# Kernel tuning notes

Measured on AMD Instinct MI355X. Metric: run time of the kernel, lower is better.

Reference implementation:

```python
import jax, jax.numpy as jnp
import numpy as np

B, T, HID = 2, 1024, 2048
H, DK, DV = 16, 128, 128
KC = 4          # short-conv kernel size
CHUNK = 64
EPS = 1e-5


def _dwconv_silu(x, w):
    # causal depthwise conv1d + SiLU: x [B,T,C], w [C,K]
    K = w.shape[1]
    xp = jnp.pad(x, ((0, 0), (K - 1, 0), (0, 0)))
    y = sum(xp[:, i:i + x.shape[1], :] * w[:, i] for i in range(K))
    return jax.nn.silu(y)


def _l2norm(x):
    return x * jax.lax.rsqrt(jnp.sum(x * x, -1, keepdims=True) + 1e-6)


def setup_inputs() -> dict:
    key = jax.random.key(0)
    ks = jax.random.split(key, 22)
    std = 0.02
    w = lambda k, s: jax.random.normal(k, s, jnp.float32) * std
    return dict(
        hidden_states=jax.random.normal(ks[0], (B, T, HID), jnp.float32),
        Wq=w(ks[1], (HID, H * DK)),
        Wk=w(ks[2], (HID, H * DK)),
        Wv=w(ks[3], (HID, H * DV)),
        conv_wq=w(ks[4], (H * DK, KC)),
        conv_wk=w(ks[5], (H * DK, KC)),
        conv_wv=w(ks[6], (H * DV, KC)),
        Wgb1=w(ks[7], (HID, DV)), Wgb2=w(ks[8], (DV, H * DK)),
        Wgd1=w(ks[9], (HID, DV)), Wgd2=w(ks[10], (DV, H * DK)),
        Wbb=w(ks[11], (HID, H)), Wbd=w(ks[12], (HID, H)),
        Wlam=w(ks[13], (HID, H)),
        A_log=jnp.log(jax.random.uniform(ks[14], (H,), jnp.float32, 1.0, 16.0)),
        dt_bias=jnp.zeros((H * DK,), jnp.float32),
        Wg1=w(ks[15], (HID, DV)), Wg2=w(ks[16], (DV, H * DV)),
        bg2=jnp.zeros((H * DV,), jnp.float32),
        onorm_w=jnp.ones((DV,), jnp.float32),
        Wo=w(ks[17], (H * DV, HID)),
    )


def _fkda_core(q, k, v, gf, gs, bf, bs):
    # dual-state (fast/slow) gated delta rule.
    # q,k: [B,T,H,DK]; v: [B,T,H,DV]; gf/gs: log-decay [B,T,H,DK]; bf/bs: [B,T,H]
    scale = DK ** -0.5
    tm = lambda x: jnp.moveaxis(x, 1, 0)                 # time-major
    qT, kT, vT = tm(q) * scale, tm(k), tm(v)
    g2 = jnp.stack([tm(gf), tm(gs)], 1)                  # [T,2,B,H,DK]
    b2 = jnp.stack([tm(bf), tm(bs)], 1)                  # [T,2,B,H]
    NC = T // CHUNK
    chunkify = lambda x: x.reshape((NC, CHUNK) + x.shape[1:])
    inputs = tuple(map(chunkify, (qT, kT, vT, g2, b2)))

    def step(S, inp):
        qt, kt, vt, gt, bt = inp                         # S: [2,B,H,DK,DV]
        S = S * jnp.exp(gt)[..., None]                   # per-channel decay on key dim
        mem = jnp.einsum('bhk,sbhkv->sbhv', kt, S)       # current memory readout
        u = bt[..., None] * (vt[None] - mem)             # delta-rule residual write
        S = S + jnp.einsum('bhk,sbhv->sbhkv', kt, u)
        o = jnp.einsum('bhk,sbhkv->sbhv', qt, S)
        return S, o

    @jax.checkpoint
    def chunk_step(S, inp):
        return jax.lax.scan(step, S, inp)

    S0 = jnp.zeros((2, q.shape[0], H, DK, DV), q.dtype)
    _, o = jax.lax.scan(chunk_step, S0, inputs)          # [NC,CHUNK,2,B,H,DV]
    o = o.reshape((T,) + o.shape[2:])
    return jnp.moveaxis(o[:, 0], 0, 1), jnp.moveaxis(o[:, 1], 0, 1)


def reference(hidden_states, Wq, Wk, Wv, conv_wq, conv_wk, conv_wv,
              Wgb1, Wgb2, Wgd1, Wgd2, Wbb, Wbd, Wlam, A_log, dt_bias,
              Wg1, Wg2, bg2, onorm_w, Wo):
    x = hidden_states
    b, t, _ = x.shape
    q = _dwconv_silu(x @ Wq, conv_wq).reshape(b, t, H, DK)
    k = _dwconv_silu(x @ Wk, conv_wk).reshape(b, t, H, DK)
    v = _dwconv_silu(x @ Wv, conv_wv).reshape(b, t, H, DV)
    g_base = ((x @ Wgb1) @ Wgb2).reshape(b, t, H, DK)    # low-rank decay gates
    g_delta = ((x @ Wgd1) @ Wgd2).reshape(b, t, H, DK)
    bb, bd = x @ Wbb, x @ Wbd
    lam = jax.nn.sigmoid(x @ Wlam)                       # [b,t,H] fast/slow mix
    beta_fast = jax.nn.sigmoid(bb + bd)
    beta_slow = jax.nn.sigmoid(bb - bd)
    dtb = dt_bias.reshape(H, DK)
    gate_of = lambda g: -jnp.exp(A_log)[None, None, :, None] * jax.nn.softplus(g + dtb)
    gf = gate_of(g_base + g_delta)                       # fused_kda_gate, fast
    gs = gate_of(g_base - g_delta)                       # slow (share_decay_gate=False)
    q, k = _l2norm(q), _l2norm(k)                        # use_qk_l2norm_in_kernel
    o_f, o_s = _fkda_core(q, k, v, gf, gs, beta_fast, beta_slow)
    o = lam[..., None] * o_f + (1.0 - lam[..., None]) * o_s
    gate = ((x @ Wg1) @ Wg2 + bg2).reshape(b, t, H, DV)
    o = o * jax.lax.rsqrt(jnp.mean(o * o, -1, keepdims=True) + EPS) * onorm_w
    o = o * jax.nn.sigmoid(gate)                         # FusedRMSNormGated(sigmoid)
    return o.reshape(b, t, H * DV) @ Wo
```

## Files before the change

kernel.cpp:

```cpp
#include <hip/hip_runtime.h>
#include <hip/hip_bf16.h>
#include <math.h>
#include <stdint.h>

#define B_   2
#define T_   1024
#define HID_ 2048
#define H_   16
#define DK_  128
#define DV_  128
#define TS_  16

typedef __bf16 bf16;
typedef __attribute__((ext_vector_type(8))) __bf16 bf16x8;
typedef __attribute__((ext_vector_type(4))) float f32x4;
typedef __attribute__((ext_vector_type(2))) float f32x2;

typedef __attribute__((address_space(3))) uint32_t* lds_ptr_t;
typedef const __attribute__((address_space(1))) uint32_t* glb_ptr_t;

__device__ __forceinline__ float sigmoidf_(float x) {
    return 1.0f / (1.0f + __expf(-x));
}

__device__ __forceinline__ void ldg_to_lds16(const void* g, void* lds) {
    __builtin_amdgcn_global_load_lds((glb_ptr_t)(uintptr_t)g,
                                     (lds_ptr_t)(uintptr_t)lds, 16, 0, 0);
}

template <int CTRL>
__device__ __forceinline__ float dpp_ror_add(float x) {
    int yi = __builtin_amdgcn_update_dpp(
        0, __builtin_bit_cast(int, x), CTRL, 0xF, 0xF, true);
    return x + __builtin_bit_cast(float, yi);
}
__device__ __forceinline__ float row16_allreduce(float x) {
    x = dpp_ror_add<0x128>(x);
    x = dpp_ror_add<0x124>(x);
    x = dpp_ror_add<0x122>(x);
    x = dpp_ror_add<0x121>(x);
    return x;
}

__global__ __launch_bounds__(256) void cast_bf16_kernel(
    const float* __restrict__ in, bf16* __restrict__ out)
{
    int i = blockIdx.x * 256 + threadIdx.x;
    float4 a = ((const float4*)in)[2 * i];
    float4 b = ((const float4*)in)[2 * i + 1];
    bf16x8 o;
    o[0] = (bf16)a.x; o[1] = (bf16)a.y; o[2] = (bf16)a.z; o[3] = (bf16)a.w;
    o[4] = (bf16)b.x; o[5] = (bf16)b.y; o[6] = (bf16)b.z; o[7] = (bf16)b.w;
    ((bf16x8*)out)[i] = o;
}

__global__ __launch_bounds__(256) void tcast_kernel(
    const float* __restrict__ W, bf16* __restrict__ Wt, int K, int N)
{
    __shared__ float tile[32][33];
    const int k0 = blockIdx.y * 32, n0 = blockIdx.x * 32;
    const int r = threadIdx.x >> 5, c = threadIdx.x & 31;
    #pragma unroll
    for (int i = 0; i < 4; ++i)
        tile[r + 8 * i][c] = W[(size_t)(k0 + r + 8 * i) * N + n0 + c];
    __syncthreads();
    #pragma unroll
    for (int i = 0; i < 4; ++i)
        Wt[(size_t)(n0 + r + 8 * i) * K + k0 + c] = (bf16)tile[c][r + 8 * i];
}

__global__ __launch_bounds__(256) void tcast_off_kernel(
    const float* __restrict__ W, bf16* __restrict__ Wt,
    int N, int noff, int koff, float sign)
{
    __shared__ float tile[32][33];
    const int k0 = blockIdx.y * 32, n0 = blockIdx.x * 32;
    const int r = threadIdx.x >> 5, c = threadIdx.x & 31;
    #pragma unroll
    for (int i = 0; i < 4; ++i)
        tile[r + 8 * i][c] = W[(size_t)(k0 + r + 8 * i) * N + n0 + c];
    __syncthreads();
    #pragma unroll
    for (int i = 0; i < 4; ++i)
        Wt[(size_t)(noff + n0 + r + 8 * i) * 256 + koff + k0 + c] =
            (bf16)(sign * tile[c][r + 8 * i]);
}

__global__ __launch_bounds__(256) void mfma_gemm_kernel(
    const bf16* __restrict__ A, const bf16* __restrict__ Bt,
    const float* __restrict__ bias, void* __restrict__ Cout,
    int M, int N, int Kfull, int lda, int ldc, int bf16out)
{
    __shared__ bf16 As[128 * 32];
    __shared__ bf16 Bs[128 * 32];

    const int tid  = threadIdx.x;
    const int w    = tid >> 6;
    const int lane = tid & 63;
    const int n0   = blockIdx.x * 128;
    const int m0   = blockIdx.y * 128;
    const int wm   = (w >> 1) * 64;
    const int wn   = (w & 1) * 64;

    const int lr = lane >> 2;
    const int lc = (lane & 3) * 8;

    f32x4 acc[4][4];
    #pragma unroll
    for (int i = 0; i < 4; ++i)
        #pragma unroll
        for (int j = 0; j < 4; ++j) acc[i][j] = (f32x4)0.0f;

    const bf16* ApL = As + (wm + (lane & 15)) * 32 + (lane >> 4) * 8;
    const bf16* BpL = Bs + (wn + (lane & 15)) * 32 + (lane >> 4) * 8;

    for (int k0 = 0; k0 < Kfull; k0 += 32) {
        #pragma unroll
        for (int i = 0; i < 2; ++i) {
            const int rr = (w * 2 + i) * 16 + lr;
            ldg_to_lds16(A  + (size_t)(m0 + rr) * lda   + k0 + lc, As + (w * 2 + i) * 512);
            ldg_to_lds16(Bt + (size_t)(n0 + rr) * Kfull + k0 + lc, Bs + (w * 2 + i) * 512);
        }
        __syncthreads();

        bf16x8 af[4], bfr[4];
        #pragma unroll
        for (int i = 0; i < 4; ++i) af[i]  = *(const bf16x8*)(ApL + i * 16 * 32);
        #pragma unroll
        for (int j = 0; j < 4; ++j) bfr[j] = *(const bf16x8*)(BpL + j * 16 * 32);
        #pragma unroll
        for (int i = 0; i < 4; ++i)
            #pragma unroll
            for (int j = 0; j < 4; ++j)
                acc[i][j] = __builtin_amdgcn_mfma_f32_16x16x32_bf16(
                    af[i], bfr[j], acc[i][j], 0, 0, 0);
        __syncthreads();
    }

    #pragma unroll
    for (int i = 0; i < 4; ++i) {
        const int row = m0 + wm + i * 16 + (lane >> 4) * 4;
        #pragma unroll
        for (int j = 0; j < 4; ++j) {
            const int col = n0 + wn + j * 16 + (lane & 15);
            const float bv = bias ? bias[col] : 0.0f;
            #pragma unroll
            for (int r = 0; r < 4; ++r) {
                float v = acc[i][j][r] + bv;
                if (bf16out) ((bf16*)Cout)[(size_t)(row + r) * ldc + col] = (bf16)v;
                else ((float*)Cout)[(size_t)(row + r) * ldc + col] = v;
            }
        }
    }
}

__global__ __launch_bounds__(256) void midcast_kernel(
    const float* __restrict__ src, bf16* __restrict__ midb)
{
    int i = blockIdx.x * 256 + threadIdx.x;
    int m = i / 96, c4 = i - m * 96;
    float4 v = *(const float4*)(src + (size_t)m * 6528 + 6144 + c4 * 4);
    bf16 o[4] = {(bf16)v.x, (bf16)v.y, (bf16)v.z, (bf16)v.w};
    *(uint64_t*)(midb + (size_t)m * 384 + c4 * 4) = *(uint64_t*)o;
}

__global__ __launch_bounds__(256) void skinny3_kernel(
    const float* __restrict__ x, const float* __restrict__ Wbb,
    const float* __restrict__ Wbd, const float* __restrict__ Wlam,
    float* __restrict__ bb, float* __restrict__ bd, float* __restrict__ lam)
{
    __shared__ float xs[16][128];
    __shared__ float wsh[128][48];
    const int m0  = blockIdx.x * 16;
    const int tid = threadIdx.x;
    const int r = tid >> 4, cg = tid & 15;
    float acc0 = 0.f, acc1 = 0.f, acc2 = 0.f;

    for (int k0 = 0; k0 < HID_; k0 += 128) {
        __syncthreads();
        #pragma unroll
        for (int i = 0; i < 2; ++i) {
            int f = tid + 256 * i;
            int rr = f >> 5, cc = (f & 31) * 4;
            *(float4*)&xs[rr][cc] = *(const float4*)(x + (size_t)(m0 + rr) * HID_ + k0 + cc);
        }
        #pragma unroll
        for (int i = 0; i < 2; ++i) {
            int f = tid + 256 * i;
            int kk = f >> 2, cc = (f & 3) * 4;
            *(float4*)&wsh[kk][cc]      = *(const float4*)(Wbb  + (size_t)(k0 + kk) * 16 + cc);
            *(float4*)&wsh[kk][16 + cc] = *(const float4*)(Wbd  + (size_t)(k0 + kk) * 16 + cc);
            *(float4*)&wsh[kk][32 + cc] = *(const float4*)(Wlam + (size_t)(k0 + kk) * 16 + cc);
        }
        __syncthreads();
        #pragma unroll 8
        for (int kk = 0; kk < 128; ++kk) {
            float xv = xs[r][kk];
            acc0 += xv * wsh[kk][cg];
            acc1 += xv * wsh[kk][16 + cg];
            acc2 += xv * wsh[kk][32 + cg];
        }
    }
    size_t o = (size_t)(m0 + r) * 16 + cg;
    bb[o] = acc0; bd[o] = acc1; lam[o] = acc2;
}

__global__ __launch_bounds__(256) void conv_silu_kernel(
    const float* __restrict__ xin, int ldx, int coloff,
    const float* __restrict__ w, float* __restrict__ yout, int mode)
{
    const int bt  = blockIdx.x;
    const int t   = bt & (T_ - 1);
    const int tid = threadIdx.x;
    const float* xr = xin + (size_t)bt * ldx + coloff;

    float val[8];
    #pragma unroll
    for (int jj = 0; jj < 8; ++jj) {
        int c = tid + 256 * jj;
        float4 wc = *(const float4*)(w + (size_t)c * 4);
        const float* xc = xr + c;
        float acc = wc.w * xc[0];
        if (t >= 1) acc += wc.z * xc[-ldx];
        if (t >= 2) acc += wc.y * xc[-2 * ldx];
        if (t >= 3) acc += wc.x * xc[-3 * ldx];
        val[jj] = acc * sigmoidf_(acc);
    }

    if (mode > 0) {
        __shared__ float red[4][8];
        const int wv = tid >> 6;
        #pragma unroll
        for (int jj = 0; jj < 8; ++jj) {
            float v2 = val[jj] * val[jj];
            #pragma unroll
            for (int m = 1; m < 64; m <<= 1) v2 += __shfl_xor(v2, m);
            if ((tid & 63) == 0) red[wv][jj] = v2;
        }
        __syncthreads();
        const int wb = (tid >> 7) * 2;
        #pragma unroll
        for (int jj = 0; jj < 8; ++jj) {
            float ss = red[wb][jj] + red[wb + 1][jj];
            float sc = rsqrtf(ss + 1e-6f);
            if (mode == 2) sc *= 0.08838834764831845f;
            val[jj] *= sc;
        }
    }

    const size_t row = (size_t)bt * HID_;
    #pragma unroll
    for (int jj = 0; jj < 8; ++jj)
        yout[row + tid + 256 * jj] = val[jj];
}

__global__ __launch_bounds__(256) void decay_gate_kernel(
    float* gfgs, const float* __restrict__ A_log,
    const float* __restrict__ dt_bias)
{
    size_t i = (size_t)blockIdx.x * 256 + threadIdx.x;
    int c = (int)(i & (HID_ - 1));
    size_t m = i >> 11;
    int h = c >> 7;
    float* pf = gfgs + m * 4096 + c;
    float* ps = pf + 2048;
    float na = -__expf(A_log[h]);
    float db = dt_bias[c];
    float xf = *pf + db;
    float xs = *ps + db;
    float spf = (xf > 20.0f) ? xf : log1pf(__expf(xf));
    float sps = (xs > 20.0f) ? xs : log1pf(__expf(xs));
    *pf = __expf(na * spf);
    *ps = __expf(na * sps);
}

__global__ __launch_bounds__(256) void fkda_kernel(
    const float* __restrict__ qp, const float* __restrict__ kp,
    const float* __restrict__ vp, const float* __restrict__ egf,
    const float* __restrict__ egs, int ldeg,
    const float* __restrict__ bbp, const float* __restrict__ bdp,
    float* __restrict__ ofp, float* __restrict__ osp)
{
    const int bx = blockIdx.x;
    const int bh = bx & 31;
    const int sv = bx >> 5;
    const int b  = bh >> 4;
    const int h  = bh & 15;
    const int s  = sv >> 3;
    const int vc = sv & 7;

    const float* eg = s ? egs : egf;
    float*       op = s ? osp : ofp;
    const float  bsign = s ? -1.0f : 1.0f;

    const int tid  = threadIdx.x;
    const int lane = tid & 63;
    const int w    = tid >> 6;
    const int kseg = lane & 15;
    const int colb = w * 4 + (lane >> 4);

    const size_t base  = (size_t)b * T_ * HID_ + (size_t)h * DK_;
    const size_t baseg = (size_t)b * T_ * ldeg + (size_t)h * DK_;
    const size_t ocol  = base + (size_t)vc * 16 + colb;

    __shared__ float EG[2][TS_ * 128];
    __shared__ float KK[2][TS_ * 128];
    __shared__ float QQ[2][TS_ * 128];
    __shared__ float VV[2][TS_ * 16];
    __shared__ float BT[2][TS_];

    f32x2 S0 = {0.f, 0.f}, S1 = {0.f, 0.f}, S2 = {0.f, 0.f}, S3 = {0.f, 0.f};

    const int l5  = lane & 31;
    const int ttl = lane >> 5;
    const int cg  = (l5 < 16) ? (l5 * 8) : ((l5 - 16) * 8 + 4);
    const int sl  = kseg * 4;

    auto stage_glds = [&](int bi, int t0) {
        #pragma unroll
        for (int i = 0; i < 2; ++i) {
            int n  = w * 2 + i;
            int tt = n * 2 + ttl;
            size_t rq = base  + (size_t)(t0 + tt) * HID_ + cg;
            size_t rg = baseg + (size_t)(t0 + tt) * ldeg + cg;
            ldg_to_lds16(eg + rg, &EG[bi][n * 256]);
            ldg_to_lds16(kp + rq, &KK[bi][n * 256]);
            ldg_to_lds16(qp + rq, &QQ[bi][n * 256]);
        }
        if (tid < 64) {
            int tt2 = tid >> 2, vo = (tid & 3) * 4;
            size_t g = base + (size_t)(t0 + tt2) * HID_ + vc * 16 + vo;
            ldg_to_lds16(vp + g, &VV[bi][0]);
        }
    };

    float bbv = 0.0f, bdv = 0.0f;
    if (tid < TS_) {
        size_t gi = ((size_t)b * T_ + tid) * H_ + h;
        bbv = bbp[gi]; bdv = bdp[gi];
    }
    stage_glds(0, 0);
    if (tid < TS_) BT[0][tid] = sigmoidf_(bbv + bsign * bdv);

    float ooPrev = 0.0f;

    for (int t0 = 0; t0 < T_; t0 += TS_) {
        const int cur = (t0 >> 4) & 1;
        const int nxt = cur ^ 1;
        const bool more = (t0 + TS_) < T_;

        __syncthreads();

        if (more) {
            stage_glds(nxt, t0 + TS_);
            if (tid < TS_) {
                size_t gi = ((size_t)b * T_ + t0 + TS_ + tid) * H_ + h;
                bbv = bbp[gi]; bdv = bdp[gi];
            }
        }

        if (t0) op[ocol + (size_t)(t0 - TS_ + kseg) * HID_] = ooPrev;

        const float* Eb = &EG[cur][sl];
        const float* Kb = &KK[cur][sl];
        const float* Qb = &QQ[cur][sl];
        const float* Vc = &VV[cur][colb];
        const float* Bc = &BT[cur][0];

        float oo = 0.0f;

        auto step = [&](const float4& ef0, const float4& ef1,
                        const float4& kf0, const float4& kf1,
                        const float4& qf0, const float4& qf1,
                        float v, float bt, int tt) {
            f32x2 e0 = {ef0.x, ef0.y}, e1 = {ef0.z, ef0.w};
            f32x2 e2 = {ef1.x, ef1.y}, e3 = {ef1.z, ef1.w};
            f32x2 k0 = {kf0.x, kf0.y}, k1 = {kf0.z, kf0.w};
            f32x2 k2 = {kf1.x, kf1.y}, k3 = {kf1.z, kf1.w};
            f32x2 q0 = {qf0.x, qf0.y}, q1 = {qf0.z, qf0.w};
            f32x2 q2 = {qf1.x, qf1.y}, q3 = {qf1.z, qf1.w};

            S0 *= e0; S1 *= e1; S2 *= e2; S3 *= e3;
            f32x2 pa = k0 * S0 + k1 * S1;
            f32x2 pb = k2 * S2 + k3 * S3;
            f32x2 ps = pa + pb;
            float p = row16_allreduce(ps.x + ps.y);

            float u = bt * (v - p);
            f32x2 u2 = {u, u};
            S0 += k0 * u2; S1 += k1 * u2; S2 += k2 * u2; S3 += k3 * u2;
            f32x2 oa = q0 * S0 + q1 * S1;
            f32x2 ob = q2 * S2 + q3 * S3;
            f32x2 om = oa + ob;
            float o = row16_allreduce(om.x + om.y);

            oo = (tt == kseg) ? o : oo;
        };

        #define LDSTEP(tt, E0, E1, K0, K1, Q0, Q1, V, BTv)          \
            E0 = *(const float4*)(Eb + (tt) * 128);                  \
            E1 = *(const float4*)(Eb + (tt) * 128 + 64);             \
            K0 = *(const float4*)(Kb + (tt) * 128);                  \
            K1 = *(const float4*)(Kb + (tt) * 128 + 64);             \
            Q0 = *(const float4*)(Qb + (tt) * 128);                  \
            Q1 = *(const float4*)(Qb + (tt) * 128 + 64);             \
            V  = Vc[(tt) * 16];                                      \
            BTv = Bc[(tt)];

        float4 eA0, eA1, kA0, kA1, qA0, qA1;
        float4 eB0, eB1, kB0, kB1, qB0, qB1;
        float  vA, btA, vB, btB;

        LDSTEP(0, eA0, eA1, kA0, kA1, qA0, qA1, vA, btA);
        #pragma unroll
        for (int tp = 0; tp < TS_; tp += 2) {
            LDSTEP(tp + 1, eB0, eB1, kB0, kB1, qB0, qB1, vB, btB);
            step(eA0, eA1, kA0, kA1, qA0, qA1, vA, btA, tp);
            if (tp + 2 < TS_) {
                LDSTEP(tp + 2, eA0, eA1, kA0, kA1, qA0, qA1, vA, btA);
            }
            step(eB0, eB1, kB0, kB1, qB0, qB1, vB, btB, tp + 1);
        }
        #undef LDSTEP

        ooPrev = oo;

        if (more && tid < TS_) BT[nxt][tid] = sigmoidf_(bbv + bsign * bdv);
    }

    op[ocol + (size_t)(T_ - TS_ + kseg) * HID_] = ooPrev;
}

__global__ __launch_bounds__(256) void mix_norm_gate_kernel(
    const float* of, const float* os, const float* lam_pre,
    const float* gate, const float* onorm_w, bf16* outp)
{
    const int bt  = blockIdx.x;
    const int tid = threadIdx.x;
    const size_t row = (size_t)bt * HID_;

    float val[8];
    #pragma unroll
    for (int jj = 0; jj < 8; ++jj) {
        int c = tid + 256 * jj;
        int h = c >> 7;
        float l = sigmoidf_(lam_pre[(size_t)bt * H_ + h]);
        val[jj] = l * of[row + c] + (1.0f - l) * os[row + c];
    }

    __shared__ float red[4][8];
    const int wv = tid >> 6;
    #pragma unroll
    for (int jj = 0; jj < 8; ++jj) {
        float v2 = val[jj] * val[jj];
        #pragma unroll
        for (int m = 1; m < 64; m <<= 1) v2 += __shfl_xor(v2, m);
        if ((tid & 63) == 0) red[wv][jj] = v2;
    }
    __syncthreads();
    const int wb = (tid >> 7) * 2;
    #pragma unroll
    for (int jj = 0; jj < 8; ++jj) {
        int c = tid + 256 * jj;
        float ss   = red[wb][jj] + red[wb + 1][jj];
        float mean = ss * (1.0f / 128.0f);
        float sc   = rsqrtf(mean + 1e-5f) * onorm_w[c & 127];
        float g    = sigmoidf_(gate[row + c]);
        outp[row + c] = (bf16)(val[jj] * sc * g);
    }
}

extern "C" void kernel_launch(void* const* d_in, const int* in_sizes, int n_in,
                              void* d_out, int out_size, void* d_ws, size_t ws_size,
                              hipStream_t stream) {
    const float* x       = (const float*)d_in[0];
    const float* Wq      = (const float*)d_in[1];
    const float* Wk      = (const float*)d_in[2];
    const float* Wv      = (const float*)d_in[3];
    const float* conv_wq = (const float*)d_in[4];
    const float* conv_wk = (const float*)d_in[5];
    const float* conv_wv = (const float*)d_in[6];
    const float* Wgb1    = (const float*)d_in[7];
    const float* Wgb2    = (const float*)d_in[8];
    const float* Wgd1    = (const float*)d_in[9];
    const float* Wgd2    = (const float*)d_in[10];
    const float* Wbb     = (const float*)d_in[11];
    const float* Wbd     = (const float*)d_in[12];
    const float* Wlam    = (const float*)d_in[13];
    const float* A_log   = (const float*)d_in[14];
    const float* dt_bias = (const float*)d_in[15];
    const float* Wg1     = (const float*)d_in[16];
    const float* Wg2     = (const float*)d_in[17];
    const float* bg2     = (const float*)d_in[18];
    const float* onorm_w = (const float*)d_in[19];
    const float* Wo      = (const float*)d_in[20];
    float* out = (float*)d_out;

    const size_t M = (size_t)B_ * T_;

    float* ws = (float*)d_ws;
    size_t off = 0;
    auto alloc = [&](size_t nfloats) { float* p = ws + off; off += nfloats; return p; };

    float* bufQKV = alloc(M * 6528);
    float* wqkvTf = alloc((size_t)6528 * HID_ / 2);
    float* xbf    = alloc(M * HID_ / 2);
    float* bufQ   = alloc(M * HID_);
    float* bufK   = alloc(M * HID_);
    float* bufV   = alloc(M * HID_);
    float* bufC   = alloc(M * HID_);
    float* bufD   = alloc(M * HID_);
    float* midbf  = alloc(M * 384 / 2);
    float* bb     = alloc(M * H_);
    float* bd     = alloc(M * H_);
    float* lamp   = alloc(M * H_);

    bf16* xb    = (bf16*)xbf;
    bf16* obf   = (bf16*)xbf;
    bf16* wqkvT = (bf16*)wqkvTf;
    bf16* woT   = wqkvT;
    bf16* wcat  = wqkvT + (size_t)HID_ * HID_;
    bf16* wgate = wcat + (size_t)4096 * 256;
    bf16* midb  = (bf16*)midbf;
    float* gfgs = bufQKV;
    float* bufE = bufQKV + M * 4096;

    dim3 blk(256);
    auto gemm = [&](const bf16* A, const bf16* Bt, const float* bias, void* C,
                    int Mm, int Nn, int Kk, int lda, int ldc, int bf16out) {
        dim3 grid(Nn / 128, Mm / 128);
        mfma_gemm_kernel<<<grid, blk, 0, stream>>>(A, Bt, bias, C, Mm, Nn, Kk,
                                                   lda, ldc, bf16out);
    };
    auto tcast = [&](const float* W, bf16* Wt, int Kk, int Nn) {
        tcast_kernel<<<dim3(Nn / 32, Kk / 32), blk, 0, stream>>>(W, Wt, Kk, Nn);
    };

    cast_bf16_kernel<<<dim3((unsigned)(M * HID_ / 8 / 256)), blk, 0, stream>>>(x, xb);

    tcast(Wq,   wqkvT,                          HID_, HID_);
    tcast(Wk,   wqkvT + (size_t)2048 * HID_,    HID_, HID_);
    tcast(Wv,   wqkvT + (size_t)4096 * HID_,    HID_, HID_);
    tcast(Wgb1, wqkvT + (size_t)6144 * HID_,    HID_, 128);
    tcast(Wgd1, wqkvT + (size_t)6272 * HID_,    HID_, 128);
    tcast(Wg1,  wqkvT + (size_t)6400 * HID_,    HID_, 128);
    gemm(xb, wqkvT, nullptr, bufQKV, (int)M, 6528, HID_, HID_, 6528, 0);

    conv_silu_kernel<<<dim3(B_ * T_), blk, 0, stream>>>(bufQKV, 6528, 0,
        conv_wq, bufQ, 2);
    conv_silu_kernel<<<dim3(B_ * T_), blk, 0, stream>>>(bufQKV, 6528, 2048,
        conv_wk, bufK, 1);
    conv_silu_kernel<<<dim3(B_ * T_), blk, 0, stream>>>(bufQKV, 6528, 4096,
        conv_wv, bufV, 0);

    midcast_kernel<<<dim3((unsigned)(M * 96 / 256)), blk, 0, stream>>>(bufQKV, midb);

    skinny3_kernel<<<dim3((unsigned)(M / 16)), blk, 0, stream>>>(
        x, Wbb, Wbd, Wlam, bb, bd, lamp);

    tcast_off_kernel<<<dim3(64, 4), blk, 0, stream>>>(Wgb2, wcat, HID_, 0,    0,   1.0f);
    tcast_off_kernel<<<dim3(64, 4), blk, 0, stream>>>(Wgd2, wcat, HID_, 0,    128, 1.0f);
    tcast_off_kernel<<<dim3(64, 4), blk, 0, stream>>>(Wgb2, wcat, HID_, 2048, 0,   1.0f);
    tcast_off_kernel<<<dim3(64, 4), blk, 0, stream>>>(Wgd2, wcat, HID_, 2048, 128, -1.0f);
    tcast(Wg2, wgate, 128, HID_);
    tcast(Wo,  woT,   HID_, HID_);
    gemm(midb,       wcat,  nullptr, gfgs, (int)M, 4096, 256, 384, 4096, 0);
    gemm(midb + 256, wgate, bg2,     bufE, (int)M, HID_, 128, 384, HID_, 0);

    decay_gate_kernel<<<dim3((unsigned)(M * HID_ / 256)), blk, 0, stream>>>(
        gfgs, A_log, dt_bias);

    fkda_kernel<<<dim3(512), blk, 0, stream>>>(bufQ, bufK, bufV,
        gfgs, gfgs + 2048, 4096, bb, bd, bufC, bufD);

    mix_norm_gate_kernel<<<dim3(B_ * T_), blk, 0, stream>>>(
        bufC, bufD, lamp, bufE, onorm_w, obf);

    gemm(obf, woT, nullptr, out, (int)M, HID_, HID_, HID_, HID_, 0);
}
```

Before: 681.7 us.

## Split recurrent state across 32 lanes per column with 512-thread blocks

The recurrence kernel now spreads each value column's key dimension over 32 lanes holding 4 state elements each, instead of 16 lanes holding 8, and doubles the block to 512 threads. Reductions gain an extra cross-half step (ds_swizzle xor-16 for the delta term, a row-broadcast DPP for the output), and staging is simplified to one load per lane. The aim is to halve per-thread serial work and register use on the latency-bound time loop. The cost is an extra cross-lane op per reduction, and only half the lanes hold valid outputs.

```diff
diff --git a/kernel.cpp b/kernel.cpp
--- a/kernel.cpp
+++ b/kernel.cpp
@@ -40,6 +40,15 @@
     x = dpp_ror_add<0x122>(x);
     x = dpp_ror_add<0x121>(x);
     return x;
+}
+__device__ __forceinline__ float xor16_add(float x) {
+    int sw = __builtin_amdgcn_ds_swizzle(__builtin_bit_cast(int, x), 0x401F);
+    return x + __builtin_bit_cast(float, sw);
+}
+__device__ __forceinline__ float bcast15_add(float x) {
+    int yi = __builtin_amdgcn_update_dpp(
+        0, __builtin_bit_cast(int, x), 0x142, 0xF, 0xF, true);
+    return x + __builtin_bit_cast(float, yi);
 }
 
 __global__ __launch_bounds__(256) void cast_bf16_kernel(
@@ -274,7 +283,7 @@
     *ps = __expf(na * sps);
 }
 
-__global__ __launch_bounds__(256) void fkda_kernel(
+__global__ __launch_bounds__(512) void fkda_kernel(
     const float* __restrict__ qp, const float* __restrict__ kp,
     const float* __restrict__ vp, const float* __restrict__ egf,
     const float* __restrict__ egs, int ldeg,
@@ -296,8 +305,8 @@
     const int tid  = threadIdx.x;
     const int lane = tid & 63;
     const int w    = tid >> 6;
-    const int kseg = lane & 15;
-    const int colb = w * 4 + (lane >> 4);
+    const int k32  = lane & 31;
+    const int colb = w * 2 + (lane >> 5);
 
     const size_t base  = (size_t)b * T_ * HID_ + (size_t)h * DK_;
     const size_t baseg = (size_t)b * T_ * ldeg + (size_t)h * DK_;
@@ -309,26 +318,21 @@
     __shared__ float VV[2][TS_ * 16];
     __shared__ float BT[2][TS_];
 
-    f32x2 S0 = {0.f, 0.f}, S1 = {0.f, 0.f}, S2 = {0.f, 0.f}, S3 = {0.f, 0.f};
-
-    const int l5  = lane & 31;
+    f32x2 S01 = {0.f, 0.f}, S23 = {0.f, 0.f};
+
     const int ttl = lane >> 5;
-    const int cg  = (l5 < 16) ? (l5 * 8) : ((l5 - 16) * 8 + 4);
-    const int sl  = kseg * 4;
+    const int cg  = k32 * 4;
+    const int sl  = cg;
 
     auto stage_glds = [&](int bi, int t0) {
-        #pragma unroll
-        for (int i = 0; i < 2; ++i) {
-            int n  = w * 2 + i;
-            int tt = n * 2 + ttl;
-            size_t rq = base  + (size_t)(t0 + tt) * HID_ + cg;
-            size_t rg = baseg + (size_t)(t0 + tt) * ldeg + cg;
-            ldg_to_lds16(eg + rg, &EG[bi][n * 256]);
-            ldg_to_lds16(kp + rq, &KK[bi][n * 256]);
-            ldg_to_lds16(qp + rq, &QQ[bi][n * 256]);
-        }
-        if (tid < 64) {
-            int tt2 = tid >> 2, vo = (tid & 3) * 4;
+        int tt = 2 * w + ttl;
+        size_t rq = base  + (size_t)(t0 + tt) * HID_ + cg;
+        size_t rg = baseg + (size_t)(t0 + tt) * ldeg + cg;
+        ldg_to_lds16(eg + rg, &EG[bi][w * 256]);
+        ldg_to_lds16(kp + rq, &KK[bi][w * 256]);
+        ldg_to_lds16(qp + rq, &QQ[bi][w * 256]);
+        if (w == 0) {
+            int tt2 = lane >> 2, vo = (lane & 3) * 4;
             size_t g = base + (size_t)(t0 + tt2) * HID_ + vc * 16 + vo;
             ldg_to_lds16(vp + g, &VV[bi][0]);
         }
@@ -359,7 +363,8 @@
             }
         }
 
-        if (t0) op[ocol + (size_t)(t0 - TS_ + kseg) * HID_] = ooPrev;
+        if (t0 && k32 >= 16)
+            op[ocol + (size_t)(t0 - TS_ + (k32 - 16)) * HID_] = ooPrev;
 
         const float* Eb = &EG[cur][sl];
         const float* Kb = &KK[cur][sl];
@@ -369,57 +374,46 @@
 
         float oo = 0.0f;
 
-        auto step = [&](const float4& ef0, const float4& ef1,
-                        const float4& kf0, const float4& kf1,
-                        const float4& qf0, const float4& qf1,
-                        float v, float bt, int tt) {
-            f32x2 e0 = {ef0.x, ef0.y}, e1 = {ef0.z, ef0.w};
-            f32x2 e2 = {ef1.x, ef1.y}, e3 = {ef1.z, ef1.w};
-            f32x2 k0 = {kf0.x, kf0.y}, k1 = {kf0.z, kf0.w};
-            f32x2 k2 = {kf1.x, kf1.y}, k3 = {kf1.z, kf1.w};
-            f32x2 q0 = {qf0.x, qf0.y}, q1 = {qf0.z, qf0.w};
-            f32x2 q2 = {qf1.x, qf1.y}, q3 = {qf1.z, qf1.w};
-
-            S0 *= e0; S1 *= e1; S2 *= e2; S3 *= e3;
-            f32x2 pa = k0 * S0 + k1 * S1;
-            f32x2 pb = k2 * S2 + k3 * S3;
-            f32x2 ps = pa + pb;
-            float p = row16_allreduce(ps.x + ps.y);
+        auto step = [&](const float4& ef, const float4& kf,
+                        const float4& qf, float v, float bt, int tt) {
+            f32x2 e01 = {ef.x, ef.y}, e23 = {ef.z, ef.w};
+            f32x2 k01 = {kf.x, kf.y}, k23 = {kf.z, kf.w};
+            f32x2 q01 = {qf.x, qf.y}, q23 = {qf.z, qf.w};
+
+            S01 *= e01; S23 *= e23;
+            f32x2 pa = k01 * S01 + k23 * S23;
+            float pp = row16_allreduce(pa.x + pa.y);
+            float p  = xor16_add(pp);
 
             float u = bt * (v - p);
             f32x2 u2 = {u, u};
-            S0 += k0 * u2; S1 += k1 * u2; S2 += k2 * u2; S3 += k3 * u2;
-            f32x2 oa = q0 * S0 + q1 * S1;
-            f32x2 ob = q2 * S2 + q3 * S3;
-            f32x2 om = oa + ob;
-            float o = row16_allreduce(om.x + om.y);
-
-            oo = (tt == kseg) ? o : oo;
+            S01 += k01 * u2; S23 += k23 * u2;
+            f32x2 oa = q01 * S01 + q23 * S23;
+            float op_ = row16_allreduce(oa.x + oa.y);
+            op_ = bcast15_add(op_);
+
+            oo = (k32 == tt + 16) ? op_ : oo;
         };
 
-        #define LDSTEP(tt, E0, E1, K0, K1, Q0, Q1, V, BTv)          \
+        #define LDSTEP(tt, E0, K0, Q0, V, BTv)                       \
             E0 = *(const float4*)(Eb + (tt) * 128);                  \
-            E1 = *(const float4*)(Eb + (tt) * 128 + 64);             \
             K0 = *(const float4*)(Kb + (tt) * 128);                  \
-            K1 = *(const float4*)(Kb + (tt) * 128 + 64);             \
             Q0 = *(const float4*)(Qb + (tt) * 128);                  \
-            Q1 = *(const float4*)(Qb + (tt) * 128 + 64);             \
             V  = Vc[(tt) * 16];                                      \
             BTv = Bc[(tt)];
 
-        float4 eA0, eA1, kA0, kA1, qA0, qA1;
-        float4 eB0, eB1, kB0, kB1, qB0, qB1;
+        float4 eA, kA, qA, eB, kB, qB;
         float  vA, btA, vB, btB;
 
-        LDSTEP(0, eA0, eA1, kA0, kA1, qA0, qA1, vA, btA);
+        LDSTEP(0, eA, kA, qA, vA, btA);
         #pragma unroll
         for (int tp = 0; tp < TS_; tp += 2) {
-            LDSTEP(tp + 1, eB0, eB1, kB0, kB1, qB0, qB1, vB, btB);
-            step(eA0, eA1, kA0, kA1, qA0, qA1, vA, btA, tp);
+            LDSTEP(tp + 1, eB, kB, qB, vB, btB);
+            step(eA, kA, qA, vA, btA, tp);
             if (tp + 2 < TS_) {
-                LDSTEP(tp + 2, eA0, eA1, kA0, kA1, qA0, qA1, vA, btA);
+                LDSTEP(tp + 2, eA, kA, qA, vA, btA);
             }
-            step(eB0, eB1, kB0, kB1, qB0, qB1, vB, btB, tp + 1);
+            step(eB, kB, qB, vB, btB, tp + 1);
         }
         #undef LDSTEP
 
@@ -428,7 +422,8 @@
         if (more && tid < TS_) BT[nxt][tid] = sigmoidf_(bbv + bsign * bdv);
     }
 
-    op[ocol + (size_t)(T_ - TS_ + kseg) * HID_] = ooPrev;
+    if (k32 >= 16)
+        op[ocol + (size_t)(T_ - TS_ + (k32 - 16)) * HID_] = ooPrev;
 }
 
 __global__ __launch_bounds__(256) void mix_norm_gate_kernel(
@@ -570,7 +565,7 @@
     decay_gate_kernel<<<dim3((unsigned)(M * HID_ / 256)), blk, 0, stream>>>(
         gfgs, A_log, dt_bias);
 
-    fkda_kernel<<<dim3(512), blk, 0, stream>>>(bufQ, bufK, bufV,
+    fkda_kernel<<<dim3(512), dim3(512), 0, stream>>>(bufQ, bufK, bufV,
         gfgs, gfgs + 2048, 4096, bb, bd, bufC, bufD);
 
     mix_norm_gate_kernel<<<dim3(B_ * T_), blk, 0, stream>>>(
```

Result: slower. 743.1 us (+9.0%).
